# Kernel optimization log

Measured on AMD Instinct MI355X. Metric: run time of the kernel, lower is better.

## Reference

```python
import jax, jax.numpy as jnp
import numpy as np

N = 50000   # nodes
E = 600000  # edges
D = 128     # input_dim == output_dim
H = 4       # heads
C = D // H  # per-head dim = 32
NEG_SLOPE = 0.2
LN_EPS = 1e-5


def setup_inputs() -> dict:
    key = jax.random.key(0)
    ks = jax.random.split(key, 6)
    s = 1.0 / np.sqrt(D)
    x = jax.random.normal(ks[0], (N, D), jnp.float32)
    edge_index = jax.random.randint(ks[1], (2, E), 0, N, dtype=jnp.int64)
    W = jax.random.normal(ks[2], (D, H * C), jnp.float32) * s          # GATConv lin (no bias)
    att_src = jax.random.normal(ks[3], (H, C), jnp.float32) * s
    att_dst = jax.random.normal(ks[4], (H, C), jnp.float32) * s
    bias = jnp.zeros((H * C,), jnp.float32)
    gamma = jnp.ones((D,), jnp.float32)   # LayerNorm weight
    beta = jnp.zeros((D,), jnp.float32)   # LayerNorm bias
    return {"x": x, "edge_index": edge_index, "W": W, "att_src": att_src,
            "att_dst": att_dst, "bias": bias, "gamma": gamma, "beta": beta}


def reference(x, edge_index, W, att_src, att_dst, bias, gamma, beta):
    n = x.shape[0]
    h = (x @ W).reshape(n, H, C)                       # [N,H,C] transformed node feats
    # PyG default add_self_loops=True
    loops = jnp.arange(n, dtype=edge_index.dtype)
    src = jnp.concatenate([edge_index[0], loops])      # message source j
    dst = jnp.concatenate([edge_index[1], loops])      # aggregation target i
    # per-node attention logits, gathered per edge
    a_src = jnp.einsum('nhc,hc->nh', h, att_src)       # [N,H]
    a_dst = jnp.einsum('nhc,hc->nh', h, att_dst)
    e = jax.nn.leaky_relu(a_src[src] + a_dst[dst], NEG_SLOPE)   # [Etot,H]
    # numerically-stable segment softmax over edges grouped by dst
    m = jax.ops.segment_max(e, dst, num_segments=n)    # every node has a self loop
    e = jnp.exp(e - m[dst])
    denom = jax.ops.segment_sum(e, dst, num_segments=n)
    alpha = e / (denom[dst] + 1e-16)                   # [Etot,H]
    # weighted scatter-add aggregation
    msg = h[src] * alpha[:, :, None]                   # [Etot,H,C]
    out = jax.ops.segment_sum(msg, dst, num_segments=n).reshape(n, H * C) + bias
    # GELU (torch default: exact erf) -> LayerNorm -> residual (dropout=identity in eval)
    f = jax.nn.gelu(out, approximate=False)
    mu = jnp.mean(f, axis=-1, keepdims=True)
    var = jnp.var(f, axis=-1, keepdims=True)
    f = (f - mu) / jnp.sqrt(var + LN_EPS) * gamma + beta
    return f + x
```

## Files before the change

kernel.cpp:

```cpp
#include <hip/hip_runtime.h>
#include <hip/hip_bf16.h>
#include <math.h>

#define DD 128
#define HH 4
#define NEG_SLOPE 0.2f
#define LN_EPS 1e-5f

typedef __attribute__((ext_vector_type(8))) short bf16x8;
typedef __attribute__((ext_vector_type(4))) float f32x4;

__device__ __forceinline__ float lrelu(float e) { return fmaxf(e, NEG_SLOPE * e); }
__device__ __forceinline__ float bflo(unsigned u) { return __uint_as_float(u << 16); }
__device__ __forceinline__ float bfhi(unsigned u) { return __uint_as_float(u & 0xFFFF0000u); }
__device__ __forceinline__ unsigned short f2bf(float f) {
    return __builtin_bit_cast(unsigned short, __float2bfloat16(f));
}


__global__ __launch_bounds__(256) void wtrans(const float* __restrict__ W,
                                              unsigned short* __restrict__ WTb) {
    __shared__ unsigned short lds[DD * DD];
    int t = threadIdx.x;
#pragma unroll
    for (int i = 0; i < 64; i++) {
        int flat = i * 256 + t;
        int k = flat >> 7, col = flat & 127;
        lds[col * DD + k] = f2bf(W[flat]);
    }
    __syncthreads();
    uint4* dst = (uint4*)WTb;
    const uint4* src = (const uint4*)lds;
#pragma unroll
    for (int i = 0; i < 8; i++) {
        int b = i * 256 + t;
        dst[b] = src[b];
    }
}


__global__ void count_kernel(const int* __restrict__ ei, int* __restrict__ deg, int E) {
    int i = blockIdx.x * blockDim.x + threadIdx.x;
    int stride = gridDim.x * blockDim.x;
    for (; i < E; i += stride) {
        atomicAdd(&deg[ei[E + i]], 1);
    }
}

__global__ __launch_bounds__(256) void partial_kernel(const int* __restrict__ deg,
                                                      int* __restrict__ bpart, int n) {
    __shared__ int r[4];
    int i = blockIdx.x * 256 + threadIdx.x;
    int v = (i < n) ? deg[i] : 0;
#pragma unroll
    for (int m = 1; m < 64; m <<= 1) v += __shfl_xor(v, m);
    if ((threadIdx.x & 63) == 0) r[threadIdx.x >> 6] = v;
    __syncthreads();
    if (threadIdx.x == 0) bpart[blockIdx.x] = r[0] + r[1] + r[2] + r[3];
}

__global__ __launch_bounds__(256) void scanpart_kernel(int* __restrict__ bpart, int nb) {
    int t = threadIdx.x;
    int v = (t < nb) ? bpart[t] : 0;
    __shared__ int ws[4];
    int x = v;
#pragma unroll
    for (int m = 1; m < 64; m <<= 1) {
        int y = __shfl_up(x, m);
        if ((t & 63) >= m) x += y;
    }
    if ((t & 63) == 63) ws[t >> 6] = x;
    __syncthreads();
    int add = 0;
    for (int w = 0; w < (t >> 6); w++) add += ws[w];
    x += add;
    if (t < nb) bpart[t] = x - v;
}

__global__ __launch_bounds__(256) void writeoff_kernel(const int* __restrict__ deg,
                                                       const int* __restrict__ bpart,
                                                       int* __restrict__ rowstart,
                                                       int* __restrict__ cursor, int n, int E) {
    int i = blockIdx.x * 256 + threadIdx.x;
    int t = threadIdx.x;
    int v = (i < n) ? deg[i] : 0;
    __shared__ int ws[4];
    int x = v;
#pragma unroll
    for (int m = 1; m < 64; m <<= 1) {
        int y = __shfl_up(x, m);
        if ((t & 63) >= m) x += y;
    }
    if ((t & 63) == 63) ws[t >> 6] = x;
    __syncthreads();
    int add = bpart[blockIdx.x];
    for (int w = 0; w < (t >> 6); w++) add += ws[w];
    int excl = x - v + add;
    if (i < n) { rowstart[i] = excl; cursor[i] = excl; }
    if (i == 0) rowstart[n] = E;
}

__global__ void fill_kernel(const int* __restrict__ ei,
                            const float* __restrict__ aS, const float* __restrict__ aD,
                            int* __restrict__ cursor, int* __restrict__ col,
                            float* __restrict__ el, int E) {
    int i = blockIdx.x * blockDim.x + threadIdx.x;
    int stride = gridDim.x * blockDim.x;
    for (; i < E; i += stride) {
        int s = ei[i];
        int d = ei[E + i];
        int pos = atomicAdd(&cursor[d], 1);
        col[pos] = s;
        float4 sv = ((const float4*)aS)[s];
        float4 dv = ((const float4*)aD)[d];
        float4 ev;
        ev.x = __expf(lrelu(sv.x + dv.x));
        ev.y = __expf(lrelu(sv.y + dv.y));
        ev.z = __expf(lrelu(sv.z + dv.z));
        ev.w = __expf(lrelu(sv.w + dv.w));
        ((float4*)el)[pos] = ev;
    }
}


__global__ __launch_bounds__(256) void gemm_mfma(const float* __restrict__ X,
                                                 const unsigned short* __restrict__ WTb,
                                                 unsigned short* __restrict__ Hb, int n) {
    __shared__ unsigned short lds[DD * DD];
    int t = threadIdx.x;
    const uint4* src = (const uint4*)WTb;
#pragma unroll
    for (int i = 0; i < 8; i++) {
        int b = i * 256 + t;
        uint4 v = src[b];
        int byteaddr = b * 16;
        int col = b >> 4;
        int swz = byteaddr ^ ((col & 15) << 4);
        *(uint4*)((char*)lds + swz) = v;
    }
    __syncthreads();

    int w = t >> 6, l = t & 63;
    int R = blockIdx.x * 64 + w * 16;
    int row = R + (l & 15);
    int rclamp = min(row, n - 1);
    int q = l >> 4;

    f32x4 acc[8];
#pragma unroll
    for (int c = 0; c < 8; c++) acc[c] = (f32x4){0.f, 0.f, 0.f, 0.f};

#pragma unroll
    for (int ks = 0; ks < 4; ks++) {
        const float* ap = X + (long)rclamp * DD + ks * 32 + q * 8;
        float4 a0 = *(const float4*)ap;
        float4 a1 = *(const float4*)(ap + 4);
        bf16x8 af;
        af[0] = (short)f2bf(a0.x); af[1] = (short)f2bf(a0.y);
        af[2] = (short)f2bf(a0.z); af[3] = (short)f2bf(a0.w);
        af[4] = (short)f2bf(a1.x); af[5] = (short)f2bf(a1.y);
        af[6] = (short)f2bf(a1.z); af[7] = (short)f2bf(a1.w);
#pragma unroll
        for (int c = 0; c < 8; c++) {
            int col = c * 16 + (l & 15);
            int byteaddr = col * 256 + ks * 64 + q * 16;
            int swz = byteaddr ^ ((col & 15) << 4);
            bf16x8 bf = *(const bf16x8*)((const char*)lds + swz);
            acc[c] = __builtin_amdgcn_mfma_f32_16x16x32_bf16(af, bf, acc[c], 0, 0, 0);
        }
    }

    int rowbase = R + q * 4;
#pragma unroll
    for (int c = 0; c < 8; c++) {
        int colw = c * 16 + (l & 15);
#pragma unroll
        for (int r = 0; r < 4; r++) {
            int orow = rowbase + r;
            if (orow < n) Hb[(long)orow * DD + colw] = f2bf(acc[c][r]);
        }
    }
}


__global__ __launch_bounds__(256) void logits_bf16(const uint4* __restrict__ Hb4,
                                                   const float* __restrict__ attS,
                                                   const float* __restrict__ attD,
                                                   float* __restrict__ aS,
                                                   float* __restrict__ aD, int n) {
    long idx = (long)blockIdx.x * 256 + threadIdx.x;
    if (idx >= (long)n * 16) return;
    int seg = (int)(idx & 15);
    int node = (int)(idx >> 4);
    int c0 = seg * 8;
    uint4 v = Hb4[idx];
    unsigned u[4] = {v.x, v.y, v.z, v.w};
    float s = 0.f, d = 0.f;
#pragma unroll
    for (int i = 0; i < 4; i++) {
        float lo = bflo(u[i]), hi = bfhi(u[i]);
        s += lo * attS[c0 + 2*i] + hi * attS[c0 + 2*i + 1];
        d += lo * attD[c0 + 2*i] + hi * attD[c0 + 2*i + 1];
    }
#pragma unroll
    for (int m = 1; m < 4; m <<= 1) {
        s += __shfl_xor(s, m);
        d += __shfl_xor(d, m);
    }
    if ((seg & 3) == 0) {
        int h = seg >> 2;
        aS[node * HH + h] = s;
        aD[node * HH + h] = d;
    }
}


__global__ __launch_bounds__(256) void agg_kernel(const unsigned* __restrict__ Hb2,
                                                  const float* __restrict__ aS,
                                                  const float* __restrict__ aD,
                                                  const float* __restrict__ el,
                                                  const int* __restrict__ rowstart,
                                                  const int* __restrict__ col,
                                                  const float* __restrict__ X,
                                                  const float* __restrict__ bias,
                                                  const float* __restrict__ gamma,
                                                  const float* __restrict__ beta,
                                                  float* __restrict__ out, int n) {
    int node = blockIdx.x * 4 + (threadIdx.x >> 6);
    if (node >= n) return;
    int lane = threadIdx.x & 63;
    int c0 = lane * 2;
    int hh = lane >> 4;

    int rs = rowstart[node];
    int re = rowstart[node + 1];

    float se = lrelu(aS[node * HH + hh] + aD[node * HH + hh]);
    float p = __expf(se);
    unsigned hv = Hb2[(long)node * 64 + lane];
    float denom = p, ax = p * bflo(hv), ay = p * bfhi(hv);
    float denom1 = 0.f, ax1 = 0.f, ay1 = 0.f;

    int k = rs;
    for (; k + 2 <= re; k += 2) {
        int j0 = col[k];
        int j1 = col[k + 1];
        float p0 = el[k * 4 + hh];
        float p1 = el[k * 4 + 4 + hh];
        unsigned g0 = Hb2[(long)j0 * 64 + lane];
        unsigned g1 = Hb2[(long)j1 * 64 + lane];
        denom  += p0; ax  += p0 * bflo(g0); ay  += p0 * bfhi(g0);
        denom1 += p1; ax1 += p1 * bflo(g1); ay1 += p1 * bfhi(g1);
    }
    if (k < re) {
        int j0 = col[k];
        float p0 = el[k * 4 + hh];
        unsigned g0 = Hb2[(long)j0 * 64 + lane];
        denom += p0; ax += p0 * bflo(g0); ay += p0 * bfhi(g0);
    }
    denom += denom1; ax += ax1; ay += ay1;

    float2 b2 = ((const float2*)bias)[lane];
    float inv = 1.0f / (denom + 1e-16f);
    float o0 = ax * inv + b2.x;
    float o1 = ay * inv + b2.y;
    float g0 = 0.5f * o0 * (1.0f + erff(o0 * 0.70710678118654752f));
    float g1 = 0.5f * o1 * (1.0f + erff(o1 * 0.70710678118654752f));

    float s1 = g0 + g1, s2 = g0 * g0 + g1 * g1;
#pragma unroll
    for (int msk = 1; msk < 64; msk <<= 1) {
        s1 += __shfl_xor(s1, msk);
        s2 += __shfl_xor(s2, msk);
    }
    float mean = s1 * (1.0f / 128.0f);
    float var = s2 * (1.0f / 128.0f) - mean * mean;
    float rstd = rsqrtf(var + LN_EPS);
    float2 gm2 = ((const float2*)gamma)[lane];
    float2 bt2 = ((const float2*)beta)[lane];
    float f0 = (g0 - mean) * rstd * gm2.x + bt2.x;
    float f1 = (g1 - mean) * rstd * gm2.y + bt2.y;

    float2 xv = ((const float2*)X)[(long)node * 64 + lane];
    float2 ov;
    ov.x = f0 + xv.x;
    ov.y = f1 + xv.y;
    ((float2*)out)[(long)node * 64 + lane] = ov;
}


extern "C" void kernel_launch(void* const* d_in, const int* in_sizes, int n_in,
                              void* d_out, int out_size, void* d_ws, size_t ws_size,
                              hipStream_t stream) {
    const float* x    = (const float*)d_in[0];
    const int*   ei   = (const int*)d_in[1];
    const float* W    = (const float*)d_in[2];
    const float* attS = (const float*)d_in[3];
    const float* attD = (const float*)d_in[4];
    const float* bias = (const float*)d_in[5];
    const float* gamma= (const float*)d_in[6];
    const float* beta = (const float*)d_in[7];
    float* out = (float*)d_out;

    int n = in_sizes[0] / DD;
    int E = in_sizes[1] / 2;
    int nb = (n + 255) / 256;

    char* ws = (char*)d_ws;
    size_t off = 0;
    auto alloc = [&](size_t bytes) -> void* {
        void* p = ws + off;
        off = (off + bytes + 255) & ~(size_t)255;
        return p;
    };
    unsigned short* Hb  = (unsigned short*)alloc((size_t)n * DD * 2);
    unsigned short* WTb = (unsigned short*)alloc((size_t)DD * DD * 2);
    float* aS       = (float*)alloc((size_t)n * HH * 4);
    float* aD       = (float*)alloc((size_t)n * HH * 4);
    int*   deg      = (int*)alloc((size_t)n * 4);
    int*   rowstart = (int*)alloc((size_t)(n + 1) * 4);
    int*   cursor   = (int*)alloc((size_t)n * 4);
    int*   col      = (int*)alloc((size_t)E * 4);
    float* el       = (float*)alloc((size_t)E * HH * 4);
    int*   bpart    = (int*)alloc((size_t)nb * 4);

    wtrans<<<1, 256, 0, stream>>>(W, WTb);
    hipMemsetAsync(deg, 0, (size_t)n * 4, stream);
    count_kernel<<<1024, 256, 0, stream>>>(ei, deg, E);
    partial_kernel<<<nb, 256, 0, stream>>>(deg, bpart, n);
    scanpart_kernel<<<1, 256, 0, stream>>>(bpart, nb);
    writeoff_kernel<<<nb, 256, 0, stream>>>(deg, bpart, rowstart, cursor, n, E);

    gemm_mfma<<<(n + 63) / 64, 256, 0, stream>>>(x, WTb, Hb, n);
    logits_bf16<<<(int)(((long)n * 16 + 255) / 256), 256, 0, stream>>>(
        (const uint4*)Hb, attS, attD, aS, aD, n);

    fill_kernel<<<1024, 256, 0, stream>>>(ei, aS, aD, cursor, col, el, E);

    agg_kernel<<<(n + 3) / 4, 256, 0, stream>>>((const unsigned*)Hb, aS, aD, el,
                                                rowstart, col, x, bias, gamma, beta, out, n);
}
```

Baseline: 224.7 us.

## Parallelize weight transpose, flatten edge kernels, precompute self-loop weights, unroll aggregation

The weight transpose is split across 8 blocks instead of running in a single block. The count and fill kernels switch from a 1024-block grid-stride loop to one thread per edge. The logits kernel now stores the exponentiated self-loop score, so the aggregation kernel no longer reads aS/aD. The aggregation loop is unrolled to four independent accumulators to keep more gathers in flight, at the cost of extra registers.

```diff
diff --git a/kernel.cpp b/kernel.cpp
--- a/kernel.cpp
+++ b/kernel.cpp
@@ -8,6 +8,7 @@
 #define LN_EPS 1e-5f
 
 typedef __attribute__((ext_vector_type(8))) short bf16x8;
+typedef __attribute__((ext_vector_type(8))) unsigned short us16x8;
 typedef __attribute__((ext_vector_type(4))) float f32x4;
 
 __device__ __forceinline__ float lrelu(float e) { return fmaxf(e, NEG_SLOPE * e); }
@@ -20,31 +21,28 @@
 
 __global__ __launch_bounds__(256) void wtrans(const float* __restrict__ W,
                                               unsigned short* __restrict__ WTb) {
-    __shared__ unsigned short lds[DD * DD];
+    __shared__ float tile[16][128];
+    int b = blockIdx.x;
     int t = threadIdx.x;
 #pragma unroll
-    for (int i = 0; i < 64; i++) {
+    for (int i = 0; i < 8; i++) {
         int flat = i * 256 + t;
-        int k = flat >> 7, col = flat & 127;
-        lds[col * DD + k] = f2bf(W[flat]);
-    }
-    __syncthreads();
-    uint4* dst = (uint4*)WTb;
-    const uint4* src = (const uint4*)lds;
-#pragma unroll
-    for (int i = 0; i < 8; i++) {
-        int b = i * 256 + t;
-        dst[b] = src[b];
-    }
-}
-
-
-__global__ void count_kernel(const int* __restrict__ ei, int* __restrict__ deg, int E) {
-    int i = blockIdx.x * blockDim.x + threadIdx.x;
-    int stride = gridDim.x * blockDim.x;
-    for (; i < E; i += stride) {
-        atomicAdd(&deg[ei[E + i]], 1);
-    }
+        int kk = flat >> 7, colc = flat & 127;
+        tile[kk][colc] = W[(b * 16 + kk) * DD + colc];
+    }
+    __syncthreads();
+    int colc = t & 127, half = t >> 7;
+    us16x8 tmp;
+#pragma unroll
+    for (int kk = 0; kk < 8; kk++) tmp[kk] = f2bf(tile[half * 8 + kk][colc]);
+    *(uint4*)&WTb[colc * DD + b * 16 + half * 8] = __builtin_bit_cast(uint4, tmp);
+}
+
+
+__global__ __launch_bounds__(256) void count_kernel(const int* __restrict__ ei,
+                                                    int* __restrict__ deg, int E) {
+    int i = blockIdx.x * 256 + threadIdx.x;
+    if (i < E) atomicAdd(&deg[ei[E + i]], 1);
 }
 
 __global__ __launch_bounds__(256) void partial_kernel(const int* __restrict__ deg,
@@ -100,26 +98,24 @@
     if (i == 0) rowstart[n] = E;
 }
 
-__global__ void fill_kernel(const int* __restrict__ ei,
+__global__ __launch_bounds__(256) void fill_kernel(const int* __restrict__ ei,
                             const float* __restrict__ aS, const float* __restrict__ aD,
                             int* __restrict__ cursor, int* __restrict__ col,
                             float* __restrict__ el, int E) {
-    int i = blockIdx.x * blockDim.x + threadIdx.x;
-    int stride = gridDim.x * blockDim.x;
-    for (; i < E; i += stride) {
-        int s = ei[i];
-        int d = ei[E + i];
-        int pos = atomicAdd(&cursor[d], 1);
-        col[pos] = s;
-        float4 sv = ((const float4*)aS)[s];
-        float4 dv = ((const float4*)aD)[d];
-        float4 ev;
-        ev.x = __expf(lrelu(sv.x + dv.x));
-        ev.y = __expf(lrelu(sv.y + dv.y));
-        ev.z = __expf(lrelu(sv.z + dv.z));
-        ev.w = __expf(lrelu(sv.w + dv.w));
-        ((float4*)el)[pos] = ev;
-    }
+    int i = blockIdx.x * 256 + threadIdx.x;
+    if (i >= E) return;
+    int s = ei[i];
+    int d = ei[E + i];
+    int pos = atomicAdd(&cursor[d], 1);
+    col[pos] = s;
+    float4 sv = ((const float4*)aS)[s];
+    float4 dv = ((const float4*)aD)[d];
+    float4 ev;
+    ev.x = __expf(lrelu(sv.x + dv.x));
+    ev.y = __expf(lrelu(sv.y + dv.y));
+    ev.z = __expf(lrelu(sv.z + dv.z));
+    ev.w = __expf(lrelu(sv.w + dv.w));
+    ((float4*)el)[pos] = ev;
 }
 
 
@@ -165,8 +161,8 @@
             int col = c * 16 + (l & 15);
             int byteaddr = col * 256 + ks * 64 + q * 16;
             int swz = byteaddr ^ ((col & 15) << 4);
-            bf16x8 bf = *(const bf16x8*)((const char*)lds + swz);
-            acc[c] = __builtin_amdgcn_mfma_f32_16x16x32_bf16(af, bf, acc[c], 0, 0, 0);
+            bf16x8 bfr = *(const bf16x8*)((const char*)lds + swz);
+            acc[c] = __builtin_amdgcn_mfma_f32_16x16x32_bf16(af, bfr, acc[c], 0, 0, 0);
         }
     }
 
@@ -187,7 +183,8 @@
                                                    const float* __restrict__ attS,
                                                    const float* __restrict__ attD,
                                                    float* __restrict__ aS,
-                                                   float* __restrict__ aD, int n) {
+                                                   float* __restrict__ aD,
+                                                   float* __restrict__ pSelf, int n) {
     long idx = (long)blockIdx.x * 256 + threadIdx.x;
     if (idx >= (long)n * 16) return;
     int seg = (int)(idx & 15);
@@ -211,13 +208,13 @@
         int h = seg >> 2;
         aS[node * HH + h] = s;
         aD[node * HH + h] = d;
+        pSelf[node * HH + h] = __expf(lrelu(s + d));
     }
 }
 
 
 __global__ __launch_bounds__(256) void agg_kernel(const unsigned* __restrict__ Hb2,
-                                                  const float* __restrict__ aS,
-                                                  const float* __restrict__ aD,
+                                                  const float* __restrict__ pSelf,
                                                   const float* __restrict__ el,
                                                   const int* __restrict__ rowstart,
                                                   const int* __restrict__ col,
@@ -235,30 +232,38 @@
     int rs = rowstart[node];
     int re = rowstart[node + 1];
 
-    float se = lrelu(aS[node * HH + hh] + aD[node * HH + hh]);
-    float p = __expf(se);
+    float p = pSelf[node * HH + hh];
     unsigned hv = Hb2[(long)node * 64 + lane];
-    float denom = p, ax = p * bflo(hv), ay = p * bfhi(hv);
-    float denom1 = 0.f, ax1 = 0.f, ay1 = 0.f;
+    float d0 = p, ax0 = p * bflo(hv), ay0 = p * bfhi(hv);
+    float d1 = 0.f, ax1 = 0.f, ay1 = 0.f;
+    float d2 = 0.f, ax2 = 0.f, ay2 = 0.f;
+    float d3 = 0.f, ax3 = 0.f, ay3 = 0.f;
 
     int k = rs;
-    for (; k + 2 <= re; k += 2) {
-        int j0 = col[k];
-        int j1 = col[k + 1];
+    for (; k + 4 <= re; k += 4) {
+        int j0 = col[k], j1 = col[k + 1], j2 = col[k + 2], j3 = col[k + 3];
         float p0 = el[k * 4 + hh];
         float p1 = el[k * 4 + 4 + hh];
+        float p2 = el[k * 4 + 8 + hh];
+        float p3 = el[k * 4 + 12 + hh];
         unsigned g0 = Hb2[(long)j0 * 64 + lane];
         unsigned g1 = Hb2[(long)j1 * 64 + lane];
-        denom  += p0; ax  += p0 * bflo(g0); ay  += p0 * bfhi(g0);
-        denom1 += p1; ax1 += p1 * bflo(g1); ay1 += p1 * bfhi(g1);
-    }
-    if (k < re) {
+        unsigned g2 = Hb2[(long)j2 * 64 + lane];
+        unsigned g3 = Hb2[(long)j3 * 64 + lane];
+        d0 += p0; ax0 += p0 * bflo(g0); ay0 += p0 * bfhi(g0);
+        d1 += p1; ax1 += p1 * bflo(g1); ay1 += p1 * bfhi(g1);
+        d2 += p2; ax2 += p2 * bflo(g2); ay2 += p2 * bfhi(g2);
+        d3 += p3; ax3 += p3 * bflo(g3); ay3 += p3 * bfhi(g3);
+    }
+    for (; k < re; k++) {
         int j0 = col[k];
         float p0 = el[k * 4 + hh];
         unsigned g0 = Hb2[(long)j0 * 64 + lane];
-        denom += p0; ax += p0 * bflo(g0); ay += p0 * bfhi(g0);
-    }
-    denom += denom1; ax += ax1; ay += ay1;
+        d0 += p0; ax0 += p0 * bflo(g0); ay0 += p0 * bfhi(g0);
+    }
+    float denom = (d0 + d1) + (d2 + d3);
+    float ax = (ax0 + ax1) + (ax2 + ax3);
+    float ay = (ay0 + ay1) + (ay2 + ay3);
 
     float2 b2 = ((const float2*)bias)[lane];
     float inv = 1.0f / (denom + 1e-16f);
@@ -305,6 +310,7 @@
     int n = in_sizes[0] / DD;
     int E = in_sizes[1] / 2;
     int nb = (n + 255) / 256;
+    int eb = (E + 255) / 256;
 
     char* ws = (char*)d_ws;
     size_t off = 0;
@@ -317,6 +323,7 @@
     unsigned short* WTb = (unsigned short*)alloc((size_t)DD * DD * 2);
     float* aS       = (float*)alloc((size_t)n * HH * 4);
     float* aD       = (float*)alloc((size_t)n * HH * 4);
+    float* pSelf    = (float*)alloc((size_t)n * HH * 4);
     int*   deg      = (int*)alloc((size_t)n * 4);
     int*   rowstart = (int*)alloc((size_t)(n + 1) * 4);
     int*   cursor   = (int*)alloc((size_t)n * 4);
@@ -324,19 +331,19 @@
     float* el       = (float*)alloc((size_t)E * HH * 4);
     int*   bpart    = (int*)alloc((size_t)nb * 4);
 
-    wtrans<<<1, 256, 0, stream>>>(W, WTb);
     hipMemsetAsync(deg, 0, (size_t)n * 4, stream);
-    count_kernel<<<1024, 256, 0, stream>>>(ei, deg, E);
+    wtrans<<<8, 256, 0, stream>>>(W, WTb);
+    count_kernel<<<eb, 256, 0, stream>>>(ei, deg, E);
     partial_kernel<<<nb, 256, 0, stream>>>(deg, bpart, n);
     scanpart_kernel<<<1, 256, 0, stream>>>(bpart, nb);
     writeoff_kernel<<<nb, 256, 0, stream>>>(deg, bpart, rowstart, cursor, n, E);
 
     gemm_mfma<<<(n + 63) / 64, 256, 0, stream>>>(x, WTb, Hb, n);
     logits_bf16<<<(int)(((long)n * 16 + 255) / 256), 256, 0, stream>>>(
-        (const uint4*)Hb, attS, attD, aS, aD, n);
-
-    fill_kernel<<<1024, 256, 0, stream>>>(ei, aS, aD, cursor, col, el, E);
-
-    agg_kernel<<<(n + 3) / 4, 256, 0, stream>>>((const unsigned*)Hb, aS, aD, el,
+        (const uint4*)Hb, attS, attD, aS, aD, pSelf, n);
+
+    fill_kernel<<<eb, 256, 0, stream>>>(ei, aS, aD, cursor, col, el, E);
+
+    agg_kernel<<<(n + 3) / 4, 256, 0, stream>>>((const unsigned*)Hb, pSelf, el,
                                                 rowstart, col, x, bias, gamma, beta, out, n);
 }
```

Result: faster. 203.7 us (-9.3%).
